# Kernel optimization log

Hardware: AMD Instinct MI355X
Metric: run time of the kernel (lower is better)

Reference implementation:

```python
import jax, jax.numpy as jnp
import numpy as np

DIM, FF, E = 1024, 4096, 8
B, S = 2, 2048


def setup_inputs() -> dict:
    key = jax.random.key(0)
    ks = jax.random.split(key, 7)
    sd = 0.02
    return {
        "x":  jax.random.normal(ks[0], (B, S, DIM), dtype=jnp.float32),
        "Wg": jax.random.normal(ks[1], (DIM, E), dtype=jnp.float32) * sd,
        "bg": jnp.zeros((E,), dtype=jnp.float32),
        "W1": jax.random.normal(ks[2], (E, DIM, FF), dtype=jnp.float32) * sd,
        "b1": jnp.zeros((E, FF), dtype=jnp.float32),
        "W2": jax.random.normal(ks[3], (E, FF, DIM), dtype=jnp.float32) * sd,
        "b2": jnp.zeros((E, DIM), dtype=jnp.float32),
    }


def reference(x, Wg, bg, W1, b1, W2, b2):
    # Gate: (B,S,E) softmax over experts
    probs = jax.nn.softmax(x @ Wg + bg, axis=-1)
    # Dense all-expert FFN (matches torch.stack over all experts), dropout is identity (eval)
    h = jax.nn.relu(jnp.einsum("bsd,edf->bsef", x, W1) + b1)        # (B,S,E,FF)
    all_out = jnp.einsum("bsef,efd->bsed", h, W2) + b2               # (B,S,E,DIM)
    # Top-2 routing, renormalized weights
    top_vals, top_idx = jax.lax.top_k(probs, 2)                      # (B,S,2)
    weights = top_vals / (jnp.sum(top_vals, axis=-1, keepdims=True) + 1e-9)
    selected = jnp.take_along_axis(all_out, top_idx[..., None], axis=2)  # (B,S,2,DIM)
    return jnp.sum(selected * weights[..., None], axis=2)            # (B,S,DIM)
```

## Files before the change

### kernel.cpp

```cpp
#include <hip/hip_runtime.h>
#include <hip/hip_bf16.h>


typedef __attribute__((ext_vector_type(8))) short bf16x8;
typedef __attribute__((ext_vector_type(4))) float f32x4;

#define MFMA16(a, b, c) __builtin_amdgcn_mfma_f32_16x16x32_bf16((a), (b), (c), 0, 0, 0)

__device__ __forceinline__ unsigned short f2bf(float f) {
  unsigned u = __builtin_bit_cast(unsigned, f);
  u += 0x7FFFu + ((u >> 16) & 1u);
  return (unsigned short)(u >> 16);
}

__device__ __forceinline__ float bf2f(unsigned short s) {
  return __builtin_bit_cast(float, (unsigned)s << 16);
}

__device__ __forceinline__ void gload_lds16(const void* g, void* l) {
  __builtin_amdgcn_global_load_lds(
      (const __attribute__((address_space(1))) unsigned int*)g,
      (__attribute__((address_space(3))) unsigned int*)l, 16, 0, 0);
}

__device__ __forceinline__ bf16x8 ldsr128(const void* p) {
  bf16x8 r;
  unsigned a = (unsigned)(unsigned long long)p;
  asm volatile("ds_read_b128 %0, %1" : "=v"(r) : "v"(a));
  return r;
}

__global__ __launch_bounds__(256) void gate_kernel(
    const float* __restrict__ x, const float* __restrict__ Wg,
    const float* __restrict__ bg, int* __restrict__ tok_e,
    float* __restrict__ tok_w, unsigned short* __restrict__ xb) {
  const int wave = threadIdx.x >> 6;
  const int lane = threadIdx.x & 63;
  const int t = blockIdx.x * 4 + wave;
  const float* xr = x + (size_t)t * 1024;
  unsigned short* xrow = xb + (size_t)t * 1024;
  double acc[8] = {0, 0, 0, 0, 0, 0, 0, 0};
  for (int i = 0; i < 16; ++i) {
    const int d = i * 64 + lane;
    const float vx = xr[d];
    xrow[d] = f2bf(vx);
    const double xv = (double)vx;
    const float* wr = Wg + d * 8;
#pragma unroll
    for (int e = 0; e < 8; ++e) acc[e] += xv * (double)wr[e];
  }
#pragma unroll
  for (int e = 0; e < 8; ++e) {
    double v = acc[e];
#pragma unroll
    for (int off = 32; off > 0; off >>= 1) v += __shfl_xor(v, off, 64);
    acc[e] = v + (double)bg[e];
  }
  if (lane == 0) {
    int e0 = 0;
#pragma unroll
    for (int e = 1; e < 8; ++e)
      if (acc[e] > acc[e0]) e0 = e;
    int e1 = (e0 == 0) ? 1 : 0;
#pragma unroll
    for (int e = 0; e < 8; ++e) {
      if (e != e0 && acc[e] > acc[e1]) e1 = e;
    }
    const double m = acc[e0];
    double s = 0.0;
#pragma unroll
    for (int e = 0; e < 8; ++e) s += exp(acc[e] - m);
    const double p0 = exp(acc[e0] - m) / s;
    const double p1 = exp(acc[e1] - m) / s;
    const double den = p0 + p1 + 1e-9;
    tok_e[2 * t] = e0;
    tok_e[2 * t + 1] = e1;
    tok_w[2 * t] = (float)(p0 / den);
    tok_w[2 * t + 1] = (float)(p1 / den);
  }
}

__global__ __launch_bounds__(256) void scan_scatter_kernel(
    const int* __restrict__ tok_e, int* __restrict__ counts,
    int* __restrict__ offsets, int* __restrict__ pair_token,
    int* __restrict__ tok_slot) {
  __shared__ int scnt[8];
  __shared__ int scur[8];
  const int tid = threadIdx.x;
  if (tid < 8) scnt[tid] = 0;
  __syncthreads();
  for (int i = tid; i < 8192; i += 256) atomicAdd(&scnt[tok_e[i]], 1);
  __syncthreads();
  if (tid == 0) {
    int s = 0;
    for (int e = 0; e < 8; ++e) {
      counts[e] = scnt[e];
      offsets[e] = s;
      scur[e] = s;
      s += scnt[e];
    }
  }
  __syncthreads();
  for (int t = tid; t < 4096; t += 256) {
#pragma unroll
    for (int j = 0; j < 2; ++j) {
      const int e = tok_e[2 * t + j];
      const int slot = atomicAdd(&scur[e], 1);
      pair_token[slot] = t;
      tok_slot[2 * t + j] = slot;
    }
  }
}

__global__ __launch_bounds__(256) void transW_kernel(
    const float* __restrict__ W1, const float* __restrict__ W2,
    unsigned short* __restrict__ W1t, unsigned short* __restrict__ W2t, int FC,
    int f0, int nW1) {
  __shared__ __align__(16) unsigned short T[64][520];
  const int tid = threadIdx.x;
  const int qi = (tid & 15) * 4;
  const int qo = (tid >> 4) * 4;

  const float* src;
  size_t srcStride;
  unsigned short* dstBase;
  size_t dstStride;

  const int bid = blockIdx.x;
  if (bid < nW1) {
    const int nf = FC / 64;
    const int e = bid / (2 * nf);
    const int rem = bid % (2 * nf);
    const int fb = (rem % nf) * 64;
    const int kb = (rem / nf) * 512;
    src = W1 + ((size_t)e * 1024 + kb) * 4096 + f0 + fb + qi;
    srcStride = 4096;
    dstBase = W1t + ((size_t)e * FC + fb) * 1024 + kb;
    dstStride = 1024;
  } else {
    const int jd = bid - nW1;
    const int nf = FC / 512;
    const int e = jd / (16 * nf);
    const int rem = jd % (16 * nf);
    const int db = (rem % 16) * 64;
    const int fbl = (rem / 16) * 512;
    src = W2 + ((size_t)e * 4096 + f0 + fbl) * 1024 + db + qi;
    srcStride = 1024;
    dstBase = W2t + ((size_t)e * 1024 + db) * FC + fbl;
    dstStride = FC;
  }

#pragma unroll
  for (int it = 0; it < 8; ++it) {
    const int o0 = it * 64 + qo;
    const float* s = src + (size_t)o0 * srcStride;
    const float4 r0 = *(const float4*)s;
    const float4 r1 = *(const float4*)(s + srcStride);
    const float4 r2 = *(const float4*)(s + 2 * srcStride);
    const float4 r3 = *(const float4*)(s + 3 * srcStride);
    uint2 u;
    u.x = (unsigned)f2bf(r0.x) | ((unsigned)f2bf(r1.x) << 16);
    u.y = (unsigned)f2bf(r2.x) | ((unsigned)f2bf(r3.x) << 16);
    *(uint2*)&T[qi + 0][o0] = u;
    u.x = (unsigned)f2bf(r0.y) | ((unsigned)f2bf(r1.y) << 16);
    u.y = (unsigned)f2bf(r2.y) | ((unsigned)f2bf(r3.y) << 16);
    *(uint2*)&T[qi + 1][o0] = u;
    u.x = (unsigned)f2bf(r0.z) | ((unsigned)f2bf(r1.z) << 16);
    u.y = (unsigned)f2bf(r2.z) | ((unsigned)f2bf(r3.z) << 16);
    *(uint2*)&T[qi + 2][o0] = u;
    u.x = (unsigned)f2bf(r0.w) | ((unsigned)f2bf(r1.w) << 16);
    u.y = (unsigned)f2bf(r2.w) | ((unsigned)f2bf(r3.w) << 16);
    *(uint2*)&T[qi + 3][o0] = u;
  }
  __syncthreads();
  const int rr = tid >> 2;
  const int sg = tid & 3;
  unsigned short* dst = dstBase + (size_t)rr * dstStride;
#pragma unroll
  for (int j = 0; j < 16; ++j) {
    const int c = sg + j * 4;
    *(uint4*)(dst + c * 8) = *(const uint4*)&T[rr][c * 8];
  }
}

#define COMPUTE64(ALDS, BLDS)                                             \
  {                                                                       \
    bf16x8 a0[4], b0[4], a1[4], b1[4];                                    \
    a0[0] = ldsr128(&ALDS[rdA[0][0]]);                                    \
    a0[1] = ldsr128(&ALDS[rdA[0][1]]);                                    \
    a0[2] = ldsr128(&ALDS[rdA[0][2]]);                                    \
    a0[3] = ldsr128(&ALDS[rdA[0][3]]);                                    \
    b0[0] = ldsr128(&BLDS[rdB[0][0]]);                                    \
    b0[1] = ldsr128(&BLDS[rdB[0][1]]);                                    \
    b0[2] = ldsr128(&BLDS[rdB[0][2]]);                                    \
    b0[3] = ldsr128(&BLDS[rdB[0][3]]);                                    \
    a1[0] = ldsr128(&ALDS[rdA[1][0]]);                                    \
    a1[1] = ldsr128(&ALDS[rdA[1][1]]);                                    \
    a1[2] = ldsr128(&ALDS[rdA[1][2]]);                                    \
    a1[3] = ldsr128(&ALDS[rdA[1][3]]);                                    \
    b1[0] = ldsr128(&BLDS[rdB[1][0]]);                                    \
    b1[1] = ldsr128(&BLDS[rdB[1][1]]);                                    \
    b1[2] = ldsr128(&BLDS[rdB[1][2]]);                                    \
    b1[3] = ldsr128(&BLDS[rdB[1][3]]);                                    \
    asm volatile("s_waitcnt lgkmcnt(8)" ::: "memory");                    \
    __builtin_amdgcn_sched_barrier(0);                                    \
    _Pragma("unroll") for (int mi = 0; mi < 4; ++mi)                      \
        _Pragma("unroll") for (int nj = 0; nj < 4; ++nj)                  \
        acc[mi][nj] = MFMA16(a0[mi], b0[nj], acc[mi][nj]);                \
    __builtin_amdgcn_sched_barrier(0);                                    \
    asm volatile("s_waitcnt lgkmcnt(0)" ::: "memory");                    \
    __builtin_amdgcn_sched_barrier(0);                                    \
    _Pragma("unroll") for (int mi = 0; mi < 4; ++mi)                      \
        _Pragma("unroll") for (int nj = 0; nj < 4; ++nj)                  \
        acc[mi][nj] = MFMA16(a1[mi], b1[nj], acc[mi][nj]);                \
    __builtin_amdgcn_sched_barrier(0);                                    \
  }

__global__ __launch_bounds__(256) void gemm1_kernel(
    const unsigned short* __restrict__ xb,
    const unsigned short* __restrict__ W1t, const float* __restrict__ b1,
    const int* __restrict__ counts, const int* __restrict__ offsets,
    const int* __restrict__ pair_token, unsigned short* __restrict__ H, int FC,
    int f0, int NT) {
  const int bid = blockIdx.x;
  const int e = bid & 7;
  const int lid = bid >> 3;
  const int n0 = (lid % NT) * 128;
  const int m0 = (lid / NT) * 128;
  const int count = counts[e];
  if (m0 >= count) return;
  const int offset = offsets[e];

  __shared__ __align__(16) unsigned short Alds[2][128 * 64];
  __shared__ __align__(16) unsigned short Blds[2][128 * 64];
  __shared__ int toklds[128];

  const int tid = threadIdx.x;
  if (tid < 128) {
    int r = m0 + tid;
    if (r >= count) r = count - 1;
    toklds[tid] = pair_token[offset + r];
  }
  __syncthreads();

  const int lane = tid & 63;
  const int wave = tid >> 6;

  const unsigned short* agp[4];
  const unsigned short* bgp[4];
  int ldso[4];
#pragma unroll
  for (int j = 0; j < 4; ++j) {
    const int g = tid + 256 * j;
    const int row = g >> 3;
    const int c = g & 7;
    const int sc = c ^ (row & 7);
    agp[j] = xb + (size_t)toklds[row] * 1024 + sc * 8;
    bgp[j] = W1t + ((size_t)e * FC + n0 + row) * 1024 + sc * 8;
    ldso[j] = (wave * 64 + 256 * j) * 8;
  }

  const int wm = (wave >> 1) * 64;
  const int wn = (wave & 1) * 64;
  const int l16 = lane & 15;
  const int lk = lane >> 4;
  int rdA[2][4], rdB[2][4];
#pragma unroll
  for (int h = 0; h < 2; ++h) {
#pragma unroll
    for (int mi = 0; mi < 4; ++mi) {
      const int row = wm + mi * 16 + l16;
      rdA[h][mi] = row * 64 + (((h * 4 + lk) ^ (row & 7)) << 3);
    }
#pragma unroll
    for (int nj = 0; nj < 4; ++nj) {
      const int row = wn + nj * 16 + l16;
      rdB[h][nj] = row * 64 + (((h * 4 + lk) ^ (row & 7)) << 3);
    }
  }

  f32x4 acc[4][4] = {};

  auto STAGE = [&](int kt, int buf) {
#pragma unroll
    for (int j = 0; j < 4; ++j) gload_lds16(agp[j] + kt * 64, &Alds[buf][ldso[j]]);
#pragma unroll
    for (int j = 0; j < 4; ++j) gload_lds16(bgp[j] + kt * 64, &Blds[buf][ldso[j]]);
  };

  const int NTk = 16;
  STAGE(0, 0);
  for (int t = 0; t < NTk; ++t) {
    __builtin_amdgcn_s_barrier();
    if (t + 1 < NTk) {
      STAGE(t + 1, (t + 1) & 1);
      asm volatile("s_waitcnt vmcnt(8)" ::: "memory");
    } else {
      asm volatile("s_waitcnt vmcnt(0)" ::: "memory");
    }
    __builtin_amdgcn_s_barrier();
    __builtin_amdgcn_sched_barrier(0);
    COMPUTE64(Alds[t & 1], Blds[t & 1]);
  }

#pragma unroll
  for (int mi = 0; mi < 4; ++mi) {
#pragma unroll
    for (int r = 0; r < 4; ++r) {
      const int rl = m0 + wm + mi * 16 + lk * 4 + r;
      if (rl >= count) continue;
      unsigned short* hrow = H + (size_t)(offset + rl) * FC;
#pragma unroll
      for (int nj = 0; nj < 4; ++nj) {
        const int c = n0 + wn + nj * 16 + l16;
        float v = acc[mi][nj][r] + b1[e * 4096 + f0 + c];
        hrow[c] = f2bf(v > 0.f ? v : 0.f);
      }
    }
  }
}

__global__ __launch_bounds__(256) void gemm2_kernel(
    const unsigned short* __restrict__ H,
    const unsigned short* __restrict__ W2t, const float* __restrict__ b2,
    const int* __restrict__ counts, const int* __restrict__ offsets,
    unsigned short* __restrict__ P, int FC, int firstChunk) {
  const int bid = blockIdx.x;
  const int e = bid & 7;
  const int r2 = bid >> 3;
  const int n0 = (r2 & 7) * 128;
  const int m0 = (r2 >> 3) * 128;
  const int count = counts[e];
  if (m0 >= count) return;
  const int offset = offsets[e];

  __shared__ __align__(16) unsigned short Alds[2][128 * 64];
  __shared__ __align__(16) unsigned short Blds[2][128 * 64];

  const int tid = threadIdx.x;
  const int lane = tid & 63;
  const int wave = tid >> 6;

  const unsigned short* agp[4];
  const unsigned short* bgp[4];
  int ldso[4];
#pragma unroll
  for (int j = 0; j < 4; ++j) {
    const int g = tid + 256 * j;
    const int row = g >> 3;
    const int c = g & 7;
    const int sc = c ^ (row & 7);
    int ar = m0 + row;
    if (ar >= count) ar = count - 1;
    agp[j] = H + (size_t)(offset + ar) * FC + sc * 8;
    bgp[j] = W2t + ((size_t)e * 1024 + n0 + row) * FC + sc * 8;
    ldso[j] = (wave * 64 + 256 * j) * 8;
  }

  const int wm = (wave >> 1) * 64;
  const int wn = (wave & 1) * 64;
  const int l16 = lane & 15;
  const int lk = lane >> 4;
  int rdA[2][4], rdB[2][4];
#pragma unroll
  for (int h = 0; h < 2; ++h) {
#pragma unroll
    for (int mi = 0; mi < 4; ++mi) {
      const int row = wm + mi * 16 + l16;
      rdA[h][mi] = row * 64 + (((h * 4 + lk) ^ (row & 7)) << 3);
    }
#pragma unroll
    for (int nj = 0; nj < 4; ++nj) {
      const int row = wn + nj * 16 + l16;
      rdB[h][nj] = row * 64 + (((h * 4 + lk) ^ (row & 7)) << 3);
    }
  }

  f32x4 acc[4][4] = {};

  auto STAGE = [&](int kt, int buf) {
#pragma unroll
    for (int j = 0; j < 4; ++j) gload_lds16(agp[j] + kt * 64, &Alds[buf][ldso[j]]);
#pragma unroll
    for (int j = 0; j < 4; ++j) gload_lds16(bgp[j] + kt * 64, &Blds[buf][ldso[j]]);
  };

  const int NTk = FC / 64;
  STAGE(0, 0);
  for (int t = 0; t < NTk; ++t) {
    __builtin_amdgcn_s_barrier();
    if (t + 1 < NTk) {
      STAGE(t + 1, (t + 1) & 1);
      asm volatile("s_waitcnt vmcnt(8)" ::: "memory");
    } else {
      asm volatile("s_waitcnt vmcnt(0)" ::: "memory");
    }
    __builtin_amdgcn_s_barrier();
    __builtin_amdgcn_sched_barrier(0);
    COMPUTE64(Alds[t & 1], Blds[t & 1]);
  }

#pragma unroll
  for (int mi = 0; mi < 4; ++mi) {
#pragma unroll
    for (int r = 0; r < 4; ++r) {
      const int rl = m0 + wm + mi * 16 + lk * 4 + r;
      if (rl >= count) continue;
      unsigned short* prow = P + (size_t)(offset + rl) * 1024;
#pragma unroll
      for (int nj = 0; nj < 4; ++nj) {
        const int c = n0 + wn + nj * 16 + l16;
        float v = acc[mi][nj][r];
        if (firstChunk) {
          prow[c] = f2bf(v + b2[e * 1024 + c]);
        } else {
          prow[c] = f2bf(bf2f(prow[c]) + v);
        }
      }
    }
  }
}

__global__ __launch_bounds__(256) void combine_kernel(
    const unsigned short* __restrict__ P, const int* __restrict__ tok_slot,
    const float* __restrict__ tok_w, float* __restrict__ out) {
  const int t = blockIdx.x;
  const int d = threadIdx.x * 4;
  const int s0 = tok_slot[2 * t];
  const int s1 = tok_slot[2 * t + 1];
  const float w0 = tok_w[2 * t];
  const float w1 = tok_w[2 * t + 1];
  const ushort4 a = *(const ushort4*)&P[(size_t)s0 * 1024 + d];
  const ushort4 b = *(const ushort4*)&P[(size_t)s1 * 1024 + d];
  float4 r;
  r.x = w0 * bf2f(a.x) + w1 * bf2f(b.x);
  r.y = w0 * bf2f(a.y) + w1 * bf2f(b.y);
  r.z = w0 * bf2f(a.z) + w1 * bf2f(b.z);
  r.w = w0 * bf2f(a.w) + w1 * bf2f(b.w);
  *(float4*)&out[(size_t)t * 1024 + d] = r;
}

extern "C" void kernel_launch(void* const* d_in, const int* in_sizes, int n_in,
                              void* d_out, int out_size, void* d_ws,
                              size_t ws_size, hipStream_t stream) {
  const float* x = (const float*)d_in[0];
  const float* Wg = (const float*)d_in[1];
  const float* bg = (const float*)d_in[2];
  const float* W1 = (const float*)d_in[3];
  const float* b1 = (const float*)d_in[4];
  const float* W2 = (const float*)d_in[5];
  const float* b2 = (const float*)d_in[6];
  float* out = (float*)d_out;

  char* w = (char*)d_ws;
  int* counts = (int*)w;
  int* offsets = counts + 16;
  int* tok_e = (int*)(w + 1024);
  float* tok_w = (float*)(w + 1024 + 32768);
  int* pair_token = (int*)(w + 1024 + 65536);
  int* tok_slot = (int*)(w + 1024 + 98304);
  unsigned short* xb = (unsigned short*)(w + 256 * 1024);
  unsigned short* P =
      (unsigned short*)(w + 256 * 1024 + 8 * 1024 * 1024);
  char* big = w + 256 * 1024 + 8 * 1024 * 1024 + 16 * 1024 * 1024;
  const size_t avail =
      ws_size - (256 * 1024 + 8 * 1024 * 1024 + 16 * 1024 * 1024);

  int FC = 4096;
  while (FC > 512 && (size_t)FC * 49152 > avail) FC >>= 1;

  unsigned short* W1t = (unsigned short*)big;
  unsigned short* W2t = W1t + (size_t)8 * FC * 1024;
  unsigned short* Hc = W2t + (size_t)8 * 1024 * FC;

  gate_kernel<<<1024, 256, 0, stream>>>(x, Wg, bg, tok_e, tok_w, xb);
  scan_scatter_kernel<<<1, 256, 0, stream>>>(tok_e, counts, offsets,
                                             pair_token, tok_slot);

  const int NT = FC / 128;
  const int nW1 = (FC / 64) * 2 * 8;
  const int nW2 = 16 * (FC / 512) * 8;
  for (int f0 = 0; f0 < 4096; f0 += FC) {
    transW_kernel<<<nW1 + nW2, 256, 0, stream>>>(W1, W2, W1t, W2t, FC, f0,
                                                 nW1);
    gemm1_kernel<<<8 * 32 * NT, 256, 0, stream>>>(
        xb, W1t, b1, counts, offsets, pair_token, Hc, FC, f0, NT);
    gemm2_kernel<<<8 * 8 * 32, 256, 0, stream>>>(
        Hc, W2t, b2, counts, offsets, P, FC, f0 == 0 ? 1 : 0);
  }
  combine_kernel<<<4096, 256, 0, stream>>>(P, tok_slot, tok_w, out);
}
```

Baseline: 333.3 us.

## Use 256x128 tiles with BK=32 and split-K gemm2 into two partial buffers

Both grouped GEMMs switch from 128x128 tiles with K-step 64 to 256x128 tiles with K-step 32. Each wave now computes a 128x64 sub-tile with 32 accumulators, which raises MFMA work per LDS read, and launch bounds request two blocks per CU. gemm2 additionally splits K into two halves that write separate P buffers, and the combine kernel sums the two halves. This keeps the gemm2 grid large despite the bigger tiles, at the cost of extra P traffic, a larger workspace, more register pressure and more tail waste on ragged per-expert counts.

```diff
diff --git a/kernel.cpp b/kernel.cpp
--- a/kernel.cpp
+++ b/kernel.cpp
@@ -183,40 +183,22 @@
   }
 }
 
-#define COMPUTE64(ALDS, BLDS)                                             \
+#define COMPUTE32(ALDS, BLDS)                                             \
   {                                                                       \
-    bf16x8 a0[4], b0[4], a1[4], b1[4];                                    \
-    a0[0] = ldsr128(&ALDS[rdA[0][0]]);                                    \
-    a0[1] = ldsr128(&ALDS[rdA[0][1]]);                                    \
-    a0[2] = ldsr128(&ALDS[rdA[0][2]]);                                    \
-    a0[3] = ldsr128(&ALDS[rdA[0][3]]);                                    \
-    b0[0] = ldsr128(&BLDS[rdB[0][0]]);                                    \
-    b0[1] = ldsr128(&BLDS[rdB[0][1]]);                                    \
-    b0[2] = ldsr128(&BLDS[rdB[0][2]]);                                    \
-    b0[3] = ldsr128(&BLDS[rdB[0][3]]);                                    \
-    a1[0] = ldsr128(&ALDS[rdA[1][0]]);                                    \
-    a1[1] = ldsr128(&ALDS[rdA[1][1]]);                                    \
-    a1[2] = ldsr128(&ALDS[rdA[1][2]]);                                    \
-    a1[3] = ldsr128(&ALDS[rdA[1][3]]);                                    \
-    b1[0] = ldsr128(&BLDS[rdB[1][0]]);                                    \
-    b1[1] = ldsr128(&BLDS[rdB[1][1]]);                                    \
-    b1[2] = ldsr128(&BLDS[rdB[1][2]]);                                    \
-    b1[3] = ldsr128(&BLDS[rdB[1][3]]);                                    \
-    asm volatile("s_waitcnt lgkmcnt(8)" ::: "memory");                    \
-    __builtin_amdgcn_sched_barrier(0);                                    \
-    _Pragma("unroll") for (int mi = 0; mi < 4; ++mi)                      \
-        _Pragma("unroll") for (int nj = 0; nj < 4; ++nj)                  \
-        acc[mi][nj] = MFMA16(a0[mi], b0[nj], acc[mi][nj]);                \
-    __builtin_amdgcn_sched_barrier(0);                                    \
+    bf16x8 a[8], b[4];                                                    \
+    _Pragma("unroll") for (int mi = 0; mi < 8; ++mi)                      \
+        a[mi] = ldsr128(&ALDS[rdA[mi]]);                                  \
+    _Pragma("unroll") for (int nj = 0; nj < 4; ++nj)                      \
+        b[nj] = ldsr128(&BLDS[rdB[nj]]);                                  \
     asm volatile("s_waitcnt lgkmcnt(0)" ::: "memory");                    \
     __builtin_amdgcn_sched_barrier(0);                                    \
-    _Pragma("unroll") for (int mi = 0; mi < 4; ++mi)                      \
+    _Pragma("unroll") for (int mi = 0; mi < 8; ++mi)                      \
         _Pragma("unroll") for (int nj = 0; nj < 4; ++nj)                  \
-        acc[mi][nj] = MFMA16(a1[mi], b1[nj], acc[mi][nj]);                \
+        acc[mi][nj] = MFMA16(a[mi], b[nj], acc[mi][nj]);                  \
     __builtin_amdgcn_sched_barrier(0);                                    \
   }
 
-__global__ __launch_bounds__(256) void gemm1_kernel(
+__global__ __launch_bounds__(256, 2) void gemm1_kernel(
     const unsigned short* __restrict__ xb,
     const unsigned short* __restrict__ W1t, const float* __restrict__ b1,
     const int* __restrict__ counts, const int* __restrict__ offsets,
@@ -226,17 +208,17 @@
   const int e = bid & 7;
   const int lid = bid >> 3;
   const int n0 = (lid % NT) * 128;
-  const int m0 = (lid / NT) * 128;
+  const int m0 = (lid / NT) * 256;
   const int count = counts[e];
   if (m0 >= count) return;
   const int offset = offsets[e];
 
-  __shared__ __align__(16) unsigned short Alds[2][128 * 64];
-  __shared__ __align__(16) unsigned short Blds[2][128 * 64];
-  __shared__ int toklds[128];
+  __shared__ __align__(16) unsigned short Alds[2][256 * 32];
+  __shared__ __align__(16) unsigned short Blds[2][128 * 32];
+  __shared__ int toklds[256];
 
   const int tid = threadIdx.x;
-  if (tid < 128) {
+  {
     int r = m0 + tid;
     if (r >= count) r = count - 1;
     toklds[tid] = pair_token[offset + r];
@@ -247,64 +229,67 @@
   const int wave = tid >> 6;
 
   const unsigned short* agp[4];
-  const unsigned short* bgp[4];
-  int ldso[4];
+  const unsigned short* bgp[2];
+  int ldsoA[4], ldsoB[2];
 #pragma unroll
   for (int j = 0; j < 4; ++j) {
     const int g = tid + 256 * j;
-    const int row = g >> 3;
-    const int c = g & 7;
-    const int sc = c ^ (row & 7);
+    const int row = g >> 2;
+    const int sc = (g & 3) ^ ((row >> 1) & 3);
     agp[j] = xb + (size_t)toklds[row] * 1024 + sc * 8;
+    ldsoA[j] = (wave * 64 + 256 * j) * 8;
+  }
+#pragma unroll
+  for (int j = 0; j < 2; ++j) {
+    const int g = tid + 256 * j;
+    const int row = g >> 2;
+    const int sc = (g & 3) ^ ((row >> 1) & 3);
     bgp[j] = W1t + ((size_t)e * FC + n0 + row) * 1024 + sc * 8;
-    ldso[j] = (wave * 64 + 256 * j) * 8;
-  }
-
-  const int wm = (wave >> 1) * 64;
+    ldsoB[j] = (wave * 64 + 256 * j) * 8;
+  }
+
+  const int wm = (wave >> 1) * 128;
   const int wn = (wave & 1) * 64;
   const int l16 = lane & 15;
   const int lk = lane >> 4;
-  int rdA[2][4], rdB[2][4];
-#pragma unroll
-  for (int h = 0; h < 2; ++h) {
-#pragma unroll
-    for (int mi = 0; mi < 4; ++mi) {
-      const int row = wm + mi * 16 + l16;
-      rdA[h][mi] = row * 64 + (((h * 4 + lk) ^ (row & 7)) << 3);
-    }
-#pragma unroll
-    for (int nj = 0; nj < 4; ++nj) {
-      const int row = wn + nj * 16 + l16;
-      rdB[h][nj] = row * 64 + (((h * 4 + lk) ^ (row & 7)) << 3);
-    }
-  }
-
-  f32x4 acc[4][4] = {};
+  int rdA[8], rdB[4];
+#pragma unroll
+  for (int mi = 0; mi < 8; ++mi) {
+    const int row = wm + mi * 16 + l16;
+    rdA[mi] = row * 32 + ((lk ^ ((row >> 1) & 3)) << 3);
+  }
+#pragma unroll
+  for (int nj = 0; nj < 4; ++nj) {
+    const int row = wn + nj * 16 + l16;
+    rdB[nj] = row * 32 + ((lk ^ ((row >> 1) & 3)) << 3);
+  }
+
+  f32x4 acc[8][4] = {};
 
   auto STAGE = [&](int kt, int buf) {
 #pragma unroll
-    for (int j = 0; j < 4; ++j) gload_lds16(agp[j] + kt * 64, &Alds[buf][ldso[j]]);
-#pragma unroll
-    for (int j = 0; j < 4; ++j) gload_lds16(bgp[j] + kt * 64, &Blds[buf][ldso[j]]);
+    for (int j = 0; j < 4; ++j) gload_lds16(agp[j] + kt, &Alds[buf][ldsoA[j]]);
+#pragma unroll
+    for (int j = 0; j < 2; ++j) gload_lds16(bgp[j] + kt, &Blds[buf][ldsoB[j]]);
   };
 
-  const int NTk = 16;
+  const int NTk = 32;
   STAGE(0, 0);
   for (int t = 0; t < NTk; ++t) {
     __builtin_amdgcn_s_barrier();
     if (t + 1 < NTk) {
-      STAGE(t + 1, (t + 1) & 1);
-      asm volatile("s_waitcnt vmcnt(8)" ::: "memory");
+      STAGE((t + 1) * 32, (t + 1) & 1);
+      asm volatile("s_waitcnt vmcnt(6)" ::: "memory");
     } else {
       asm volatile("s_waitcnt vmcnt(0)" ::: "memory");
     }
     __builtin_amdgcn_s_barrier();
     __builtin_amdgcn_sched_barrier(0);
-    COMPUTE64(Alds[t & 1], Blds[t & 1]);
-  }
-
-#pragma unroll
-  for (int mi = 0; mi < 4; ++mi) {
+    COMPUTE32(Alds[t & 1], Blds[t & 1]);
+  }
+
+#pragma unroll
+  for (int mi = 0; mi < 8; ++mi) {
 #pragma unroll
     for (int r = 0; r < 4; ++r) {
       const int rl = m0 + wm + mi * 16 + lk * 4 + r;
@@ -320,7 +305,7 @@
   }
 }
 
-__global__ __launch_bounds__(256) void gemm2_kernel(
+__global__ __launch_bounds__(256, 2) void gemm2_kernel(
     const unsigned short* __restrict__ H,
     const unsigned short* __restrict__ W2t, const float* __restrict__ b2,
     const int* __restrict__ counts, const int* __restrict__ offsets,
@@ -329,90 +314,98 @@
   const int e = bid & 7;
   const int r2 = bid >> 3;
   const int n0 = (r2 & 7) * 128;
-  const int m0 = (r2 >> 3) * 128;
+  const int m0 = ((r2 >> 3) & 15) * 256;
+  const int ks = r2 >> 7;
   const int count = counts[e];
   if (m0 >= count) return;
   const int offset = offsets[e];
-
-  __shared__ __align__(16) unsigned short Alds[2][128 * 64];
-  __shared__ __align__(16) unsigned short Blds[2][128 * 64];
+  const int KS = FC / 2;
+  const int kb = ks * KS;
+  unsigned short* Pb = P + (size_t)ks * 8192 * 1024;
+
+  __shared__ __align__(16) unsigned short Alds[2][256 * 32];
+  __shared__ __align__(16) unsigned short Blds[2][128 * 32];
 
   const int tid = threadIdx.x;
   const int lane = tid & 63;
   const int wave = tid >> 6;
 
   const unsigned short* agp[4];
-  const unsigned short* bgp[4];
-  int ldso[4];
+  const unsigned short* bgp[2];
+  int ldsoA[4], ldsoB[2];
 #pragma unroll
   for (int j = 0; j < 4; ++j) {
     const int g = tid + 256 * j;
-    const int row = g >> 3;
-    const int c = g & 7;
-    const int sc = c ^ (row & 7);
+    const int row = g >> 2;
+    const int sc = (g & 3) ^ ((row >> 1) & 3);
     int ar = m0 + row;
     if (ar >= count) ar = count - 1;
-    agp[j] = H + (size_t)(offset + ar) * FC + sc * 8;
-    bgp[j] = W2t + ((size_t)e * 1024 + n0 + row) * FC + sc * 8;
-    ldso[j] = (wave * 64 + 256 * j) * 8;
-  }
-
-  const int wm = (wave >> 1) * 64;
+    agp[j] = H + (size_t)(offset + ar) * FC + kb + sc * 8;
+    ldsoA[j] = (wave * 64 + 256 * j) * 8;
+  }
+#pragma unroll
+  for (int j = 0; j < 2; ++j) {
+    const int g = tid + 256 * j;
+    const int row = g >> 2;
+    const int sc = (g & 3) ^ ((row >> 1) & 3);
+    bgp[j] = W2t + ((size_t)e * 1024 + n0 + row) * FC + kb + sc * 8;
+    ldsoB[j] = (wave * 64 + 256 * j) * 8;
+  }
+
+  const int wm = (wave >> 1) * 128;
   const int wn = (wave & 1) * 64;
   const int l16 = lane & 15;
   const int lk = lane >> 4;
-  int rdA[2][4], rdB[2][4];
-#pragma unroll
-  for (int h = 0; h < 2; ++h) {
-#pragma unroll
-    for (int mi = 0; mi < 4; ++mi) {
-      const int row = wm + mi * 16 + l16;
-      rdA[h][mi] = row * 64 + (((h * 4 + lk) ^ (row & 7)) << 3);
-    }
-#pragma unroll
-    for (int nj = 0; nj < 4; ++nj) {
-      const int row = wn + nj * 16 + l16;
-      rdB[h][nj] = row * 64 + (((h * 4 + lk) ^ (row & 7)) << 3);
-    }
-  }
-
-  f32x4 acc[4][4] = {};
+  int rdA[8], rdB[4];
+#pragma unroll
+  for (int mi = 0; mi < 8; ++mi) {
+    const int row = wm + mi * 16 + l16;
+    rdA[mi] = row * 32 + ((lk ^ ((row >> 1) & 3)) << 3);
+  }
+#pragma unroll
+  for (int nj = 0; nj < 4; ++nj) {
+    const int row = wn + nj * 16 + l16;
+    rdB[nj] = row * 32 + ((lk ^ ((row >> 1) & 3)) << 3);
+  }
+
+  f32x4 acc[8][4] = {};
 
   auto STAGE = [&](int kt, int buf) {
 #pragma unroll
-    for (int j = 0; j < 4; ++j) gload_lds16(agp[j] + kt * 64, &Alds[buf][ldso[j]]);
-#pragma unroll
-    for (int j = 0; j < 4; ++j) gload_lds16(bgp[j] + kt * 64, &Blds[buf][ldso[j]]);
+    for (int j = 0; j < 4; ++j) gload_lds16(agp[j] + kt, &Alds[buf][ldsoA[j]]);
+#pragma unroll
+    for (int j = 0; j < 2; ++j) gload_lds16(bgp[j] + kt, &Blds[buf][ldsoB[j]]);
   };
 
-  const int NTk = FC / 64;
+  const int NTk = KS / 32;
   STAGE(0, 0);
   for (int t = 0; t < NTk; ++t) {
     __builtin_amdgcn_s_barrier();
     if (t + 1 < NTk) {
-      STAGE(t + 1, (t + 1) & 1);
-      asm volatile("s_waitcnt vmcnt(8)" ::: "memory");
+      STAGE((t + 1) * 32, (t + 1) & 1);
+      asm volatile("s_waitcnt vmcnt(6)" ::: "memory");
     } else {
       asm volatile("s_waitcnt vmcnt(0)" ::: "memory");
     }
     __builtin_amdgcn_s_barrier();
     __builtin_amdgcn_sched_barrier(0);
-    COMPUTE64(Alds[t & 1], Blds[t & 1]);
-  }
-
-#pragma unroll
-  for (int mi = 0; mi < 4; ++mi) {
+    COMPUTE32(Alds[t & 1], Blds[t & 1]);
+  }
+
+#pragma unroll
+  for (int mi = 0; mi < 8; ++mi) {
 #pragma unroll
     for (int r = 0; r < 4; ++r) {
       const int rl = m0 + wm + mi * 16 + lk * 4 + r;
       if (rl >= count) continue;
-      unsigned short* prow = P + (size_t)(offset + rl) * 1024;
+      unsigned short* prow = Pb + (size_t)(offset + rl) * 1024;
 #pragma unroll
       for (int nj = 0; nj < 4; ++nj) {
         const int c = n0 + wn + nj * 16 + l16;
         float v = acc[mi][nj][r];
+        if (ks == 0 && firstChunk) v += b2[e * 1024 + c];
         if (firstChunk) {
-          prow[c] = f2bf(v + b2[e * 1024 + c]);
+          prow[c] = f2bf(v);
         } else {
           prow[c] = f2bf(bf2f(prow[c]) + v);
         }
@@ -430,13 +423,15 @@
   const int s1 = tok_slot[2 * t + 1];
   const float w0 = tok_w[2 * t];
   const float w1 = tok_w[2 * t + 1];
-  const ushort4 a = *(const ushort4*)&P[(size_t)s0 * 1024 + d];
-  const ushort4 b = *(const ushort4*)&P[(size_t)s1 * 1024 + d];
+  const ushort4 a0 = *(const ushort4*)&P[(size_t)s0 * 1024 + d];
+  const ushort4 a1 = *(const ushort4*)&P[(size_t)(8192 + s0) * 1024 + d];
+  const ushort4 c0 = *(const ushort4*)&P[(size_t)s1 * 1024 + d];
+  const ushort4 c1 = *(const ushort4*)&P[(size_t)(8192 + s1) * 1024 + d];
   float4 r;
-  r.x = w0 * bf2f(a.x) + w1 * bf2f(b.x);
-  r.y = w0 * bf2f(a.y) + w1 * bf2f(b.y);
-  r.z = w0 * bf2f(a.z) + w1 * bf2f(b.z);
-  r.w = w0 * bf2f(a.w) + w1 * bf2f(b.w);
+  r.x = w0 * (bf2f(a0.x) + bf2f(a1.x)) + w1 * (bf2f(c0.x) + bf2f(c1.x));
+  r.y = w0 * (bf2f(a0.y) + bf2f(a1.y)) + w1 * (bf2f(c0.y) + bf2f(c1.y));
+  r.z = w0 * (bf2f(a0.z) + bf2f(a1.z)) + w1 * (bf2f(c0.z) + bf2f(c1.z));
+  r.w = w0 * (bf2f(a0.w) + bf2f(a1.w)) + w1 * (bf2f(c0.w) + bf2f(c1.w));
   *(float4*)&out[(size_t)t * 1024 + d] = r;
 }
 
@@ -462,9 +457,9 @@
   unsigned short* xb = (unsigned short*)(w + 256 * 1024);
   unsigned short* P =
       (unsigned short*)(w + 256 * 1024 + 8 * 1024 * 1024);
-  char* big = w + 256 * 1024 + 8 * 1024 * 1024 + 16 * 1024 * 1024;
+  char* big = w + 256 * 1024 + 8 * 1024 * 1024 + 32 * 1024 * 1024;
   const size_t avail =
-      ws_size - (256 * 1024 + 8 * 1024 * 1024 + 16 * 1024 * 1024);
+      ws_size - (256 * 1024 + 8 * 1024 * 1024 + 32 * 1024 * 1024);
 
   int FC = 4096;
   while (FC > 512 && (size_t)FC * 49152 > avail) FC >>= 1;
@@ -483,9 +478,9 @@
   for (int f0 = 0; f0 < 4096; f0 += FC) {
     transW_kernel<<<nW1 + nW2, 256, 0, stream>>>(W1, W2, W1t, W2t, FC, f0,
                                                  nW1);
-    gemm1_kernel<<<8 * 32 * NT, 256, 0, stream>>>(
+    gemm1_kernel<<<8 * 16 * NT, 256, 0, stream>>>(
         xb, W1t, b1, counts, offsets, pair_token, Hc, FC, f0, NT);
-    gemm2_kernel<<<8 * 8 * 32, 256, 0, stream>>>(
+    gemm2_kernel<<<8 * 8 * 16 * 2, 256, 0, stream>>>(
         Hc, W2t, b2, counts, offsets, P, FC, f0 == 0 ? 1 : 0);
   }
   combine_kernel<<<4096, 256, 0, stream>>>(P, tok_slot, tok_w, out);
```

Result: no change. 333.3 us (-0.0%).
